# Optimization experiments

Measured on AMD Instinct MI355X. Metric: run time of the kernel, lower is better.

Reference implementation:

```python
import jax, jax.numpy as jnp
import numpy as np

N = 2_097_152
NUM_DIM = 4
NUM_FACTOR = 32
VOCABS = {"dow": 7, "time": 24, "sex": 2, "age": 100, "month": 12, "day": 31}
NUM_DEST = 100_000


def setup_inputs() -> dict:
    key = jax.random.key(0)
    ks = jax.random.split(key, 16)
    inp = {}
    # forward index args
    names = ["dayofweek", "time", "sex", "age", "month", "day"]
    maxes = [7, 24, 2, 100, 12, 31]
    for i, (n, m) in enumerate(zip(names, maxes)):
        inp[n] = jax.random.randint(ks[i], (N,), 0, m, dtype=jnp.int64 if jax.config.jax_enable_x64 else jnp.int32)
    inp["destination"] = jax.random.randint(ks[6], (N,), 0, NUM_DEST, dtype=jnp.int32)
    # learned params (all feature embeddings ~ N(0,1) like nn.init.normal_)
    inp["emb_dow"] = jax.random.normal(ks[7], (7, NUM_DIM), jnp.float32)
    inp["emb_time"] = jax.random.normal(ks[8], (24, NUM_DIM), jnp.float32)
    inp["emb_sex"] = jax.random.normal(ks[9], (2, NUM_DIM), jnp.float32)
    inp["emb_age"] = jax.random.normal(ks[10], (100, NUM_DIM), jnp.float32)
    inp["emb_month"] = jax.random.normal(ks[11], (12, NUM_DIM), jnp.float32)
    inp["emb_day"] = jax.random.normal(ks[12], (31, NUM_DIM), jnp.float32)
    # user projection Linear(6*num_dim -> num_factor)
    fan_in = 6 * NUM_DIM
    bound = 1.0 / np.sqrt(fan_in)
    inp["W"] = jax.random.uniform(ks[13], (fan_in, NUM_FACTOR), jnp.float32, -bound, bound)
    inp["b"] = jax.random.uniform(ks[14], (NUM_FACTOR,), jnp.float32, -bound, bound)
    inp["item_table"] = jax.random.normal(ks[15], (NUM_DEST, NUM_FACTOR), jnp.float32)
    return inp


def reference(dayofweek, time, sex, age, month, day, destination,
              emb_dow, emb_time, emb_sex, emb_age, emb_month, emb_day,
              W, b, item_table):
    # user embedding: gather 6 feature embeddings, concat -> [N, 24], project -> [N, 32]
    u = jnp.concatenate([
        emb_dow[dayofweek], emb_time[time], emb_sex[sex],
        emb_age[age], emb_month[month], emb_day[day],
    ], axis=-1)
    user = u @ W + b                      # [N, F]
    item = item_table[destination]        # [N, F]
    # diag(user @ item^T) == row-wise dot product (same math, O(N) not O(N^2))
    return jnp.sum(user * item, axis=-1)  # [N]
```

## Files before the change

### kernel.cpp

```cpp
#include <hip/hip_runtime.h>


#define NF 32
#define LDS_STRIDE 36
#define NV2 323
#define T1_OFF 168
#define T2_OFF 192
#define T3_OFF 292

__device__ __forceinline__ float4 ldsf4(const float* p) {
    return *reinterpret_cast<const float4*>(p);
}

__device__ __forceinline__ float dot4(float4 u, float4 v, float a) {
    a = fmaf(u.x, v.x, a);
    a = fmaf(u.y, v.y, a);
    a = fmaf(u.z, v.z, a);
    a = fmaf(u.w, v.w, a);
    return a;
}

#define QUAD(IV, Q)                                                  \
    acc0 = dot4(ldsf4(&proj[b0 + (Q) * 4]), IV, acc0);               \
    acc1 = dot4(ldsf4(&proj[b1 + (Q) * 4]), IV, acc1);               \
    acc2 = dot4(ldsf4(&proj[b2 + (Q) * 4]), IV, acc2);               \
    acc3 = dot4(ldsf4(&proj[b3 + (Q) * 4]), IV, acc3);

#define NTL(P) __builtin_nontemporal_load(P)

__global__ __launch_bounds__(512, 6)
void mf_kernel(const int* __restrict__ dow, const int* __restrict__ tmi,
               const int* __restrict__ sx,  const int* __restrict__ ag,
               const int* __restrict__ mo,  const int* __restrict__ dy,
               const int* __restrict__ dst,
               const float* __restrict__ e_dow,   const float* __restrict__ e_time,
               const float* __restrict__ e_sex,   const float* __restrict__ e_age,
               const float* __restrict__ e_month, const float* __restrict__ e_day,
               const float* __restrict__ W, const float* __restrict__ bvec,
               const float* __restrict__ item_table,
               float* __restrict__ out, int n)
{
    __shared__ float proj[NV2 * LDS_STRIDE];

    const int tid = threadIdx.x;
    for (int t = tid; t < NV2 * NF; t += blockDim.x) {
        const int entry = t >> 5;
        const int f     = t & 31;
        float acc;
        if (entry < T1_OFF) {
            const int a = entry / 24;
            const int b = entry - a * 24;
            acc = bvec[f];
            #pragma unroll
            for (int d = 0; d < 4; ++d) {
                acc = fmaf(e_dow[a * 4 + d],  W[(0  + d) * NF + f], acc);
                acc = fmaf(e_time[b * 4 + d], W[(4  + d) * NF + f], acc);
            }
        } else if (entry < T2_OFF) {
            const int e2 = entry - T1_OFF;
            const int a = e2 / 12;
            const int b = e2 - a * 12;
            acc = 0.0f;
            #pragma unroll
            for (int d = 0; d < 4; ++d) {
                acc = fmaf(e_sex[a * 4 + d],   W[(8  + d) * NF + f], acc);
                acc = fmaf(e_month[b * 4 + d], W[(16 + d) * NF + f], acc);
            }
        } else if (entry < T3_OFF) {
            const int v = entry - T2_OFF;
            acc = 0.0f;
            #pragma unroll
            for (int d = 0; d < 4; ++d)
                acc = fmaf(e_age[v * 4 + d], W[(12 + d) * NF + f], acc);
        } else {
            const int v = entry - T3_OFF;
            acc = 0.0f;
            #pragma unroll
            for (int d = 0; d < 4; ++d)
                acc = fmaf(e_day[v * 4 + d], W[(20 + d) * NF + f], acc);
        }
        proj[entry * LDS_STRIDE + f] = acc;
    }
    __syncthreads();

    const int tstride = gridDim.x * blockDim.x;
    int i = blockIdx.x * blockDim.x + tid;
    if (i >= n) return;

    int j0 = NTL(&dow[i]), j1 = NTL(&tmi[i]), j2 = NTL(&sx[i]),
        j3 = NTL(&ag[i]),  j4 = NTL(&mo[i]),  j5 = NTL(&dy[i]),
        jd = NTL(&dst[i]);

    for (;;) {
        const int b0 = (j0 * 24 + j1) * LDS_STRIDE;
        const int b1 = (T1_OFF + j2 * 12 + j4) * LDS_STRIDE;
        const int b2 = (T2_OFF + j3) * LDS_STRIDE;
        const int b3 = (T3_OFF + j5) * LDS_STRIDE;
        const float4* it = reinterpret_cast<const float4*>(item_table + (long long)jd * NF);

        float4 iv0 = it[0];
        float4 iv1 = it[1];
        float4 iv2 = it[2];
        float4 iv3 = it[3];
        float4 iv4 = it[4];
        float4 iv5 = it[5];
        float4 iv6 = it[6];
        float4 iv7 = it[7];

        const int ni = i + tstride;
        const bool more = ni < n;
        if (more) {
            j0 = NTL(&dow[ni]); j1 = NTL(&tmi[ni]); j2 = NTL(&sx[ni]);
            j3 = NTL(&ag[ni]);  j4 = NTL(&mo[ni]);  j5 = NTL(&dy[ni]);
            jd = NTL(&dst[ni]);
        }

        asm volatile("" ::: "memory");

        float acc0 = 0.0f, acc1 = 0.0f, acc2 = 0.0f, acc3 = 0.0f;
        QUAD(iv0, 0)
        QUAD(iv1, 1)
        QUAD(iv2, 2)
        QUAD(iv3, 3)
        QUAD(iv4, 4)
        QUAD(iv5, 5)
        QUAD(iv6, 6)
        QUAD(iv7, 7)
        __builtin_nontemporal_store((acc0 + acc1) + (acc2 + acc3), &out[i]);

        if (!more) break;
        i = ni;
    }
}

extern "C" void kernel_launch(void* const* d_in, const int* in_sizes, int n_in,
                              void* d_out, int out_size, void* d_ws, size_t ws_size,
                              hipStream_t stream) {
    const int* dow = (const int*)d_in[0];
    const int* tmi = (const int*)d_in[1];
    const int* sx  = (const int*)d_in[2];
    const int* ag  = (const int*)d_in[3];
    const int* mo  = (const int*)d_in[4];
    const int* dy  = (const int*)d_in[5];
    const int* dst = (const int*)d_in[6];
    const float* e_dow   = (const float*)d_in[7];
    const float* e_time  = (const float*)d_in[8];
    const float* e_sex   = (const float*)d_in[9];
    const float* e_age   = (const float*)d_in[10];
    const float* e_month = (const float*)d_in[11];
    const float* e_day   = (const float*)d_in[12];
    const float* W       = (const float*)d_in[13];
    const float* bvec    = (const float*)d_in[14];
    const float* item    = (const float*)d_in[15];
    float* out = (float*)d_out;
    const int n = in_sizes[0];

    dim3 grid(1024), block(512);
    mf_kernel<<<grid, block, 0, stream>>>(dow, tmi, sx, ag, mo, dy, dst,
                                          e_dow, e_time, e_sex, e_age, e_month, e_day,
                                          W, bvec, item, out, n);
}
```

Measured before the change: 187.8 us.

## Shrink projected LDS table and double-buffer item rows across iterations

Changes the precomputed projection table from 4 groups (dow×time, sex×month, age, day) to 5 groups (dow×sex, time, age, month, day). This shrinks LDS from 323 to 181 rows, which lowers the setup cost per block and leaves room for more resident blocks. The cost is one extra LDS float4 read per quad. The main loop becomes a two-stage software pipeline: the item-table row for the next element is loaded while the current one is computed, and indices are prefetched two iterations ahead. Launch shape changes to 1280 blocks of 256 threads with matching launch bounds, at the price of more registers held by the double-buffered rows.

```diff
diff --git a/kernel.cpp b/kernel.cpp
--- a/kernel.cpp
+++ b/kernel.cpp
@@ -3,10 +3,11 @@
 
 #define NF 32
 #define LDS_STRIDE 36
-#define NV2 323
-#define T1_OFF 168
-#define T2_OFF 192
-#define T3_OFF 292
+#define NV 181
+#define T1_OFF 14
+#define T2_OFF 38
+#define T3_OFF 138
+#define T4_OFF 150
 
 __device__ __forceinline__ float4 ldsf4(const float* p) {
     return *reinterpret_cast<const float4*>(p);
@@ -20,15 +21,51 @@
     return a;
 }
 
+#define NTL(P) __builtin_nontemporal_load(P)
+
+struct IdxSet { int j0, j1, j2, j3, j4, j5, jd; };
+struct RowSet { float4 q0, q1, q2, q3, q4, q5, q6, q7; };
+
 #define QUAD(IV, Q)                                                  \
     acc0 = dot4(ldsf4(&proj[b0 + (Q) * 4]), IV, acc0);               \
     acc1 = dot4(ldsf4(&proj[b1 + (Q) * 4]), IV, acc1);               \
     acc2 = dot4(ldsf4(&proj[b2 + (Q) * 4]), IV, acc2);               \
-    acc3 = dot4(ldsf4(&proj[b3 + (Q) * 4]), IV, acc3);
+    acc0 = dot4(ldsf4(&proj[b3 + (Q) * 4]), IV, acc0);               \
+    acc1 = dot4(ldsf4(&proj[b4 + (Q) * 4]), IV, acc1);
 
-#define NTL(P) __builtin_nontemporal_load(P)
+#define LOAD_IDX(J, I)                                               \
+    J.j0 = NTL(&dow[I]); J.j1 = NTL(&tmi[I]); J.j2 = NTL(&sx[I]);    \
+    J.j3 = NTL(&ag[I]);  J.j4 = NTL(&mo[I]);  J.j5 = NTL(&dy[I]);    \
+    J.jd = NTL(&dst[I]);
 
-__global__ __launch_bounds__(512, 6)
+#define LOAD_ROW(R, JD)                                              \
+    {                                                                \
+        const float4* itp = reinterpret_cast<const float4*>(         \
+            item_table + (long long)(JD) * NF);                      \
+        R.q0 = itp[0]; R.q1 = itp[1]; R.q2 = itp[2]; R.q3 = itp[3];  \
+        R.q4 = itp[4]; R.q5 = itp[5]; R.q6 = itp[6]; R.q7 = itp[7];  \
+    }
+
+#define STEP(RC, RN, JC, JN, ICUR, INXT)                                   \
+    {                                                                      \
+        const int b0 = (JC.j2 * 7 + JC.j0)   * LDS_STRIDE;                 \
+        const int b1 = (T1_OFF + JC.j1)      * LDS_STRIDE;                 \
+        const int b2 = (T2_OFF + JC.j3)      * LDS_STRIDE;                 \
+        const int b3 = (T3_OFF + JC.j4)      * LDS_STRIDE;                 \
+        const int b4 = (T4_OFF + JC.j5)      * LDS_STRIDE;                 \
+        if ((INXT) < n) {                                                  \
+            LOAD_ROW(RN, JN.jd)                                            \
+            const int i3 = (INXT) + tstride;                              \
+            if (i3 < n) { LOAD_IDX(JC, i3) }                               \
+        }                                                                  \
+        asm volatile("" ::: "memory");                                     \
+        float acc0 = 0.0f, acc1 = 0.0f, acc2 = 0.0f;                       \
+        QUAD(RC.q0, 0) QUAD(RC.q1, 1) QUAD(RC.q2, 2) QUAD(RC.q3, 3)        \
+        QUAD(RC.q4, 4) QUAD(RC.q5, 5) QUAD(RC.q6, 6) QUAD(RC.q7, 7)        \
+        __builtin_nontemporal_store(acc0 + acc1 + acc2, &out[ICUR]);       \
+    }
+
+__global__ __launch_bounds__(256, 5)
 void mf_kernel(const int* __restrict__ dow, const int* __restrict__ tmi,
                const int* __restrict__ sx,  const int* __restrict__ ag,
                const int* __restrict__ mo,  const int* __restrict__ dy,
@@ -40,40 +77,42 @@
                const float* __restrict__ item_table,
                float* __restrict__ out, int n)
 {
-    __shared__ float proj[NV2 * LDS_STRIDE];
+    __shared__ float proj[NV * LDS_STRIDE];
 
     const int tid = threadIdx.x;
-    for (int t = tid; t < NV2 * NF; t += blockDim.x) {
+    for (int t = tid; t < NV * NF; t += blockDim.x) {
         const int entry = t >> 5;
         const int f     = t & 31;
         float acc;
         if (entry < T1_OFF) {
-            const int a = entry / 24;
-            const int b = entry - a * 24;
+            const int s  = entry / 7;
+            const int d0 = entry - s * 7;
             acc = bvec[f];
             #pragma unroll
             for (int d = 0; d < 4; ++d) {
-                acc = fmaf(e_dow[a * 4 + d],  W[(0  + d) * NF + f], acc);
-                acc = fmaf(e_time[b * 4 + d], W[(4  + d) * NF + f], acc);
+                acc = fmaf(e_dow[d0 * 4 + d], W[(0 + d) * NF + f], acc);
+                acc = fmaf(e_sex[s * 4 + d],  W[(8 + d) * NF + f], acc);
             }
         } else if (entry < T2_OFF) {
-            const int e2 = entry - T1_OFF;
-            const int a = e2 / 12;
-            const int b = e2 - a * 12;
+            const int v = entry - T1_OFF;
             acc = 0.0f;
             #pragma unroll
-            for (int d = 0; d < 4; ++d) {
-                acc = fmaf(e_sex[a * 4 + d],   W[(8  + d) * NF + f], acc);
-                acc = fmaf(e_month[b * 4 + d], W[(16 + d) * NF + f], acc);
-            }
+            for (int d = 0; d < 4; ++d)
+                acc = fmaf(e_time[v * 4 + d], W[(4 + d) * NF + f], acc);
         } else if (entry < T3_OFF) {
             const int v = entry - T2_OFF;
             acc = 0.0f;
             #pragma unroll
             for (int d = 0; d < 4; ++d)
                 acc = fmaf(e_age[v * 4 + d], W[(12 + d) * NF + f], acc);
+        } else if (entry < T4_OFF) {
+            const int v = entry - T3_OFF;
+            acc = 0.0f;
+            #pragma unroll
+            for (int d = 0; d < 4; ++d)
+                acc = fmaf(e_month[v * 4 + d], W[(16 + d) * NF + f], acc);
         } else {
-            const int v = entry - T3_OFF;
+            const int v = entry - T4_OFF;
             acc = 0.0f;
             #pragma unroll
             for (int d = 0; d < 4; ++d)
@@ -87,49 +126,21 @@
     int i = blockIdx.x * blockDim.x + tid;
     if (i >= n) return;
 
-    int j0 = NTL(&dow[i]), j1 = NTL(&tmi[i]), j2 = NTL(&sx[i]),
-        j3 = NTL(&ag[i]),  j4 = NTL(&mo[i]),  j5 = NTL(&dy[i]),
-        jd = NTL(&dst[i]);
+    IdxSet P, Q;
+    RowSet A, B;
+
+    LOAD_IDX(P, i)
+    LOAD_ROW(A, P.jd)
+    int i2 = i + tstride;
+    if (i2 < n) { LOAD_IDX(Q, i2) }
 
     for (;;) {
-        const int b0 = (j0 * 24 + j1) * LDS_STRIDE;
-        const int b1 = (T1_OFF + j2 * 12 + j4) * LDS_STRIDE;
-        const int b2 = (T2_OFF + j3) * LDS_STRIDE;
-        const int b3 = (T3_OFF + j5) * LDS_STRIDE;
-        const float4* it = reinterpret_cast<const float4*>(item_table + (long long)jd * NF);
-
-        float4 iv0 = it[0];
-        float4 iv1 = it[1];
-        float4 iv2 = it[2];
-        float4 iv3 = it[3];
-        float4 iv4 = it[4];
-        float4 iv5 = it[5];
-        float4 iv6 = it[6];
-        float4 iv7 = it[7];
-
-        const int ni = i + tstride;
-        const bool more = ni < n;
-        if (more) {
-            j0 = NTL(&dow[ni]); j1 = NTL(&tmi[ni]); j2 = NTL(&sx[ni]);
-            j3 = NTL(&ag[ni]);  j4 = NTL(&mo[ni]);  j5 = NTL(&dy[ni]);
-            jd = NTL(&dst[ni]);
-        }
-
-        asm volatile("" ::: "memory");
-
-        float acc0 = 0.0f, acc1 = 0.0f, acc2 = 0.0f, acc3 = 0.0f;
-        QUAD(iv0, 0)
-        QUAD(iv1, 1)
-        QUAD(iv2, 2)
-        QUAD(iv3, 3)
-        QUAD(iv4, 4)
-        QUAD(iv5, 5)
-        QUAD(iv6, 6)
-        QUAD(iv7, 7)
-        __builtin_nontemporal_store((acc0 + acc1) + (acc2 + acc3), &out[i]);
-
-        if (!more) break;
-        i = ni;
+        STEP(A, B, P, Q, i, i2)
+        if (i2 >= n) break;
+        i = i2; i2 += tstride;
+        STEP(B, A, Q, P, i, i2)
+        if (i2 >= n) break;
+        i = i2; i2 += tstride;
     }
 }
 
@@ -155,7 +166,7 @@
     float* out = (float*)d_out;
     const int n = in_sizes[0];
 
-    dim3 grid(1024), block(512);
+    dim3 grid(1280), block(256);
     mf_kernel<<<grid, block, 0, stream>>>(dow, tmi, sx, ag, mo, dy, dst,
                                           e_dow, e_time, e_sex, e_age, e_month, e_day,
                                           W, bvec, item, out, n);
```

Result: slower. 274.9 us (+46.3%).

## Shrink LDS projection table to five smaller tables to raise occupancy

Applied to the files above, without the earlier changes.

Reorganizes the precomputed per-feature projection tables in LDS from four tables (323 entries, pairing dow×time and sex×month) to five tables (181 entries, pairing only dow×sex). This cuts LDS use per block and the precompute work, so launch bounds are raised from 6 to 8 blocks per CU. The trade is five LDS float4 gathers per quad instead of four, which adds LDS traffic and FMAs in the main loop.

```diff
diff --git a/kernel.cpp b/kernel.cpp
--- a/kernel.cpp
+++ b/kernel.cpp
@@ -3,10 +3,11 @@
 
 #define NF 32
 #define LDS_STRIDE 36
-#define NV2 323
-#define T1_OFF 168
-#define T2_OFF 192
-#define T3_OFF 292
+#define NV 181
+#define T1_OFF 14
+#define T2_OFF 38
+#define T3_OFF 138
+#define T4_OFF 150
 
 __device__ __forceinline__ float4 ldsf4(const float* p) {
     return *reinterpret_cast<const float4*>(p);
@@ -24,11 +25,12 @@
     acc0 = dot4(ldsf4(&proj[b0 + (Q) * 4]), IV, acc0);               \
     acc1 = dot4(ldsf4(&proj[b1 + (Q) * 4]), IV, acc1);               \
     acc2 = dot4(ldsf4(&proj[b2 + (Q) * 4]), IV, acc2);               \
-    acc3 = dot4(ldsf4(&proj[b3 + (Q) * 4]), IV, acc3);
+    acc0 = dot4(ldsf4(&proj[b3 + (Q) * 4]), IV, acc0);               \
+    acc1 = dot4(ldsf4(&proj[b4 + (Q) * 4]), IV, acc1);
 
 #define NTL(P) __builtin_nontemporal_load(P)
 
-__global__ __launch_bounds__(512, 6)
+__global__ __launch_bounds__(512, 8)
 void mf_kernel(const int* __restrict__ dow, const int* __restrict__ tmi,
                const int* __restrict__ sx,  const int* __restrict__ ag,
                const int* __restrict__ mo,  const int* __restrict__ dy,
@@ -40,40 +42,42 @@
                const float* __restrict__ item_table,
                float* __restrict__ out, int n)
 {
-    __shared__ float proj[NV2 * LDS_STRIDE];
+    __shared__ float proj[NV * LDS_STRIDE];
 
     const int tid = threadIdx.x;
-    for (int t = tid; t < NV2 * NF; t += blockDim.x) {
+    for (int t = tid; t < NV * NF; t += blockDim.x) {
         const int entry = t >> 5;
         const int f     = t & 31;
         float acc;
         if (entry < T1_OFF) {
-            const int a = entry / 24;
-            const int b = entry - a * 24;
+            const int s  = entry / 7;
+            const int d0 = entry - s * 7;
             acc = bvec[f];
             #pragma unroll
             for (int d = 0; d < 4; ++d) {
-                acc = fmaf(e_dow[a * 4 + d],  W[(0  + d) * NF + f], acc);
-                acc = fmaf(e_time[b * 4 + d], W[(4  + d) * NF + f], acc);
+                acc = fmaf(e_dow[d0 * 4 + d], W[(0 + d) * NF + f], acc);
+                acc = fmaf(e_sex[s * 4 + d],  W[(8 + d) * NF + f], acc);
             }
         } else if (entry < T2_OFF) {
-            const int e2 = entry - T1_OFF;
-            const int a = e2 / 12;
-            const int b = e2 - a * 12;
+            const int v = entry - T1_OFF;
             acc = 0.0f;
             #pragma unroll
-            for (int d = 0; d < 4; ++d) {
-                acc = fmaf(e_sex[a * 4 + d],   W[(8  + d) * NF + f], acc);
-                acc = fmaf(e_month[b * 4 + d], W[(16 + d) * NF + f], acc);
-            }
+            for (int d = 0; d < 4; ++d)
+                acc = fmaf(e_time[v * 4 + d], W[(4 + d) * NF + f], acc);
         } else if (entry < T3_OFF) {
             const int v = entry - T2_OFF;
             acc = 0.0f;
             #pragma unroll
             for (int d = 0; d < 4; ++d)
                 acc = fmaf(e_age[v * 4 + d], W[(12 + d) * NF + f], acc);
+        } else if (entry < T4_OFF) {
+            const int v = entry - T3_OFF;
+            acc = 0.0f;
+            #pragma unroll
+            for (int d = 0; d < 4; ++d)
+                acc = fmaf(e_month[v * 4 + d], W[(16 + d) * NF + f], acc);
         } else {
-            const int v = entry - T3_OFF;
+            const int v = entry - T4_OFF;
             acc = 0.0f;
             #pragma unroll
             for (int d = 0; d < 4; ++d)
@@ -92,10 +96,11 @@
         jd = NTL(&dst[i]);
 
     for (;;) {
-        const int b0 = (j0 * 24 + j1) * LDS_STRIDE;
-        const int b1 = (T1_OFF + j2 * 12 + j4) * LDS_STRIDE;
-        const int b2 = (T2_OFF + j3) * LDS_STRIDE;
-        const int b3 = (T3_OFF + j5) * LDS_STRIDE;
+        const int b0 = (j2 * 7 + j0)      * LDS_STRIDE;
+        const int b1 = (T1_OFF + j1)      * LDS_STRIDE;
+        const int b2 = (T2_OFF + j3)      * LDS_STRIDE;
+        const int b3 = (T3_OFF + j4)      * LDS_STRIDE;
+        const int b4 = (T4_OFF + j5)      * LDS_STRIDE;
         const float4* it = reinterpret_cast<const float4*>(item_table + (long long)jd * NF);
 
         float4 iv0 = it[0];
@@ -117,7 +122,7 @@
 
         asm volatile("" ::: "memory");
 
-        float acc0 = 0.0f, acc1 = 0.0f, acc2 = 0.0f, acc3 = 0.0f;
+        float acc0 = 0.0f, acc1 = 0.0f, acc2 = 0.0f;
         QUAD(iv0, 0)
         QUAD(iv1, 1)
         QUAD(iv2, 2)
@@ -126,7 +131,7 @@
         QUAD(iv5, 5)
         QUAD(iv6, 6)
         QUAD(iv7, 7)
-        __builtin_nontemporal_store((acc0 + acc1) + (acc2 + acc3), &out[i]);
+        __builtin_nontemporal_store(acc0 + acc1 + acc2, &out[i]);
 
         if (!more) break;
         i = ni;
```

Result: faster. 167.5 us (-10.8%).
